# Kernel tuning notes

Measured on AMD Instinct MI355X. Metric: run time of the kernel, lower is better.

## Reference

```python
import jax, jax.numpy as jnp
import numpy as np

N_NODES = 100000
N_EDGES = 3200000
F_IN, HID, N_CLS = 512, 16, 40


def setup_inputs() -> dict:
    key = jax.random.key(0)
    ks = jax.random.split(key, 7)
    x = jax.random.normal(ks[0], (N_NODES, F_IN), dtype=jnp.float32)
    edge_index = jax.random.randint(ks[1], (2, N_EDGES), 0, N_NODES, dtype=jnp.int32)
    edge_weight = jax.random.uniform(ks[2], (N_EDGES,), dtype=jnp.float32)
    # Glorot-style init like PyG's Linear inside GCNConv
    W1 = jax.random.normal(ks[3], (F_IN, HID), dtype=jnp.float32) * (1.0 / np.sqrt(F_IN))
    b1 = jnp.zeros((HID,), dtype=jnp.float32)
    W2 = jax.random.normal(ks[4], (HID, N_CLS), dtype=jnp.float32) * (1.0 / np.sqrt(HID))
    b2 = jnp.zeros((N_CLS,), dtype=jnp.float32)
    return {"x": x, "edge_index": edge_index, "edge_weight": edge_weight,
            "W1": W1, "b1": b1, "W2": W2, "b2": b2}


def reference(x, edge_index, edge_weight, W1, b1, W2, b2):
    N = x.shape[0]
    src, dst = edge_index[0], edge_index[1]
    # add self-loops with weight 1 (GCNConv default add_self_loops=True)
    loop = jnp.arange(N, dtype=edge_index.dtype)
    src_f = jnp.concatenate([src, loop])
    dst_f = jnp.concatenate([dst, loop])
    ew_f = jnp.concatenate([edge_weight, jnp.ones((N,), dtype=edge_weight.dtype)])
    # symmetric normalization: deg computed over target nodes (source_to_target flow)
    deg = jax.ops.segment_sum(ew_f, dst_f, num_segments=N)
    dis = jnp.where(deg > 0, jax.lax.rsqrt(jnp.where(deg > 0, deg, 1.0)), 0.0)
    norm = dis[src_f] * ew_f * dis[dst_f]  # [E+N]

    def conv(h, W, b):
        h = h @ W  # linear before propagate, as in PyG GCNConv
        msg = h[src_f] * norm[:, None]  # [E+N, d_out]
        agg = jax.ops.segment_sum(msg, dst_f, num_segments=N)
        return agg + b

    h = jax.nn.relu(conv(x, W1, b1))
    # dropout is identity in eval mode
    out = conv(h, W2, b2)
    return jax.nn.log_softmax(out, axis=1)
```

## Files before the change

kernel.cpp:

```cpp
#include <hip/hip_runtime.h>
#include <hip/hip_bf16.h>

constexpr int F_IN  = 512;
constexpr int HID   = 16;
constexpr int NCLS  = 40;
constexpr int CHUNK = 4096;
constexpr int BMAX  = 800;
constexpr int SMAX  = 6144;

__device__ __forceinline__ unsigned packEdge(int s, float w) {
  __hip_bfloat16 h = __float2bfloat16(w);
  unsigned short hb = *reinterpret_cast<unsigned short*>(&h);
  return ((unsigned)s << 15) | (unsigned)(hb & 0x7fff);
}
__device__ __forceinline__ float edgeW(unsigned p) {
  return __uint_as_float((p & 0x7fffu) << 16);
}

__global__ void k_scanA(const int* __restrict__ a, int* __restrict__ bsum, int valid) {
  __shared__ int sd[256];
  int t = threadIdx.x;
  int i4 = blockIdx.x * 256 + t;
  int4 v = reinterpret_cast<const int4*>(a)[i4];
  int base = i4 * 4;
  int s = ((base + 0 < valid) ? v.x : 0) + ((base + 1 < valid) ? v.y : 0) +
          ((base + 2 < valid) ? v.z : 0) + ((base + 3 < valid) ? v.w : 0);
  sd[t] = s; __syncthreads();
  for (int off = 128; off > 0; off >>= 1) {
    if (t < off) sd[t] += sd[t + off];
    __syncthreads();
  }
  if (!t) bsum[blockIdx.x] = sd[0];
}

__global__ void k_scanB(int* __restrict__ bsum, int nb) {
  __shared__ int sd[1024];
  int t = threadIdx.x;
  int v = (t < nb) ? bsum[t] : 0;
  sd[t] = v;
  __syncthreads();
  for (int off = 1; off < 1024; off <<= 1) {
    int add = (t >= off) ? sd[t - off] : 0;
    __syncthreads();
    sd[t] += add;
    __syncthreads();
  }
  if (t < nb) bsum[t] = sd[t] - v;
}

__global__ void k_scanC(int* __restrict__ a, const int* __restrict__ bsum, int valid) {
  __shared__ int sd[256];
  int t = threadIdx.x;
  int i4 = blockIdx.x * 256 + t;
  int4 v = reinterpret_cast<int4*>(a)[i4];
  int base = i4 * 4;
  int vx = (base + 0 < valid) ? v.x : 0;
  int vy = (base + 1 < valid) ? v.y : 0;
  int vz = (base + 2 < valid) ? v.z : 0;
  int vw = (base + 3 < valid) ? v.w : 0;
  int ts = vx + vy + vz + vw;
  sd[t] = ts;
  __syncthreads();
  for (int off = 1; off < 256; off <<= 1) {
    int add = (t >= off) ? sd[t - off] : 0;
    __syncthreads();
    sd[t] += add;
    __syncthreads();
  }
  int pre = bsum[blockIdx.x] + sd[t] - ts;
  int4 w;
  w.x = pre; w.y = pre + vx; w.z = w.y + vy; w.w = w.z + vz;
  reinterpret_cast<int4*>(a)[i4] = w;
}

__global__ void __launch_bounds__(256)
k_scat2(const int* __restrict__ src, const int* __restrict__ dst,
        const float* __restrict__ ew, unsigned* __restrict__ payloadA,
        unsigned char* __restrict__ dlowA, int* __restrict__ segs,
        int* __restrict__ counts, int E, int NB, int NBLK) {
  __shared__ unsigned ebuf32[CHUNK];
  __shared__ unsigned char ebufd[CHUNK];
  __shared__ int hist[1024];
  __shared__ int sc[256];
  int t = threadIdx.x;
  int c = blockIdx.x;
  int cbase = c * CHUNK;
  int sz = min(CHUNK, E - cbase);
#pragma unroll
  for (int i = 0; i < 4; ++i) hist[t + 256 * i] = 0;
  __syncthreads();
  unsigned pk[16];
  unsigned char dl[16];
  int key[16];
#pragma unroll
  for (int r = 0; r < 16; ++r) {
    int i = r * 256 + t;
    int e = cbase + i;
    if (i < sz) {
      int s = src[e], d = dst[e];
      pk[r] = packEdge(s, ew[e]);
      dl[r] = (unsigned char)(d & 127);
      key[r] = d >> 7;
      atomicAdd(&hist[key[r]], 1);
    } else {
      key[r] = -1;
    }
  }
  __syncthreads();
  int h0 = hist[4 * t], h1 = hist[4 * t + 1], h2 = hist[4 * t + 2], h3 = hist[4 * t + 3];
  int tsum = h0 + h1 + h2 + h3;
  sc[t] = tsum;
  __syncthreads();
  for (int off = 1; off < 256; off <<= 1) {
    int add = (t >= off) ? sc[t - off] : 0;
    __syncthreads();
    sc[t] += add;
    __syncthreads();
  }
  int pre = sc[t] - tsum;
  __syncthreads();
  hist[4 * t]     = pre;
  hist[4 * t + 1] = pre + h0;
  hist[4 * t + 2] = pre + h0 + h1;
  hist[4 * t + 3] = pre + h0 + h1 + h2;
  __syncthreads();
  size_t sb = (size_t)c * (NB + 1);
  for (int b = t; b < NB; b += 256) {
    int lo = hist[b];
    segs[sb + b] = lo;
    counts[b * NBLK + c] = hist[b + 1] - lo;
  }
  if (t == 0) segs[sb + NB] = sz;
  __syncthreads();
#pragma unroll
  for (int r = 0; r < 16; ++r) {
    if (key[r] >= 0) {
      int pos = atomicAdd(&hist[key[r]], 1);
      ebuf32[pos] = pk[r];
      ebufd[pos]  = dl[r];
    }
  }
  __syncthreads();
  for (int i = t; i < sz; i += 256) {
    payloadA[cbase + i] = ebuf32[i];
    dlowA[cbase + i]    = ebufd[i];
  }
}

__global__ void __launch_bounds__(256)
k_sortb2(const unsigned* __restrict__ payloadA, const unsigned char* __restrict__ dlowA,
         const int* __restrict__ segs, const int* __restrict__ cnts,
         unsigned* __restrict__ payloadB, int* __restrict__ rs,
         float* __restrict__ dis, int N, int NB, int NBLK) {
  __shared__ unsigned ebuf32[SMAX];
  __shared__ unsigned char ebufd[SMAX];
  __shared__ int hcnt[128];
  __shared__ int scn[128];
  __shared__ float dgs[128];
  int t = threadIdx.x;
  int b = blockIdx.x;
  if (t < 128) { hcnt[t] = 0; dgs[t] = 1.0f; }
  __syncthreads();
  int beg = cnts[b * NBLK];
  int end = cnts[b * NBLK + NBLK];
  for (int c = t; c < NBLK; c += 256) {
    int rel = cnts[b * NBLK + c] - beg;
    size_t sb = (size_t)c * (NB + 1) + b;
    int s0 = segs[sb], s1 = segs[sb + 1];
    int gsrc = c * CHUNK + s0;
    for (int k = 0; k < s1 - s0; ++k) {
      unsigned p = payloadA[gsrc + k];
      unsigned char d8 = dlowA[gsrc + k];
      ebuf32[rel + k] = p;
      ebufd[rel + k]  = d8;
      atomicAdd(&hcnt[d8], 1);
      atomicAdd(&dgs[d8], edgeW(p));
    }
  }
  __syncthreads();
  int v = (t < 128) ? hcnt[t] : 0;
  if (t < 128) scn[t] = v;
  __syncthreads();
  for (int off = 1; off < 128; off <<= 1) {
    int add = (t < 128 && t >= off) ? scn[t - off] : 0;
    __syncthreads();
    if (t < 128) scn[t] += add;
    __syncthreads();
  }
  int base = b * 128;
  if (t < 128) {
    int st = scn[t] - v;
    hcnt[t] = st;
    rs[base + t] = beg + st;
    int n = base + t;
    if (n < N) dis[n] = rsqrtf(dgs[t]);
  }
  if (t == 0) rs[base + 128] = end;
  __syncthreads();
  int sz = end - beg;
  for (int i = t; i < sz; i += 256) {
    int pos = beg + atomicAdd(&hcnt[ebufd[i]], 1);
    payloadB[pos] = ebuf32[i];
  }
}

__device__ __forceinline__ float blo(unsigned u) { return __uint_as_float(u << 16); }
__device__ __forceinline__ float bhi(unsigned u) { return __uint_as_float(u & 0xffff0000u); }
__device__ __forceinline__ unsigned pack2(float lo, float hi) {
  __hip_bfloat16 l = __float2bfloat16(lo), h = __float2bfloat16(hi);
  unsigned short ul = *reinterpret_cast<unsigned short*>(&l);
  unsigned short uh = *reinterpret_cast<unsigned short*>(&h);
  return (unsigned)ul | ((unsigned)uh << 16);
}

__global__ void __launch_bounds__(256)
k_gemm1f(const float* __restrict__ x, const float* __restrict__ W1,
         const float* __restrict__ dis, uint4* __restrict__ hb1, int N) {
  __shared__ unsigned xs[4352];
  int t = threadIdx.x;
  int nb = blockIdx.x * 64;
  int r = t & 63;
  int sId = __builtin_amdgcn_readfirstlane(t >> 6);
  float2 acc[8];
#pragma unroll
  for (int j2 = 0; j2 < 8; ++j2) acc[j2] = make_float2(0.f, 0.f);

  float4 ld0, ld1, ld2, ld3, ld4, ld5, ld6, ld7;
#define G1F_LOAD(c)                                                          \
  do {                                                                       \
    int f;                                                                   \
    f = t;           { int row = f >> 5, sl = f & 31; int n = nb + row;      \
      ld0 = (n < N) ? *reinterpret_cast<const float4*>(x + (size_t)n * F_IN + (c) * 128 + sl * 4) : make_float4(0,0,0,0); } \
    f = t + 256;     { int row = f >> 5, sl = f & 31; int n = nb + row;      \
      ld1 = (n < N) ? *reinterpret_cast<const float4*>(x + (size_t)n * F_IN + (c) * 128 + sl * 4) : make_float4(0,0,0,0); } \
    f = t + 512;     { int row = f >> 5, sl = f & 31; int n = nb + row;      \
      ld2 = (n < N) ? *reinterpret_cast<const float4*>(x + (size_t)n * F_IN + (c) * 128 + sl * 4) : make_float4(0,0,0,0); } \
    f = t + 768;     { int row = f >> 5, sl = f & 31; int n = nb + row;      \
      ld3 = (n < N) ? *reinterpret_cast<const float4*>(x + (size_t)n * F_IN + (c) * 128 + sl * 4) : make_float4(0,0,0,0); } \
    f = t + 1024;    { int row = f >> 5, sl = f & 31; int n = nb + row;      \
      ld4 = (n < N) ? *reinterpret_cast<const float4*>(x + (size_t)n * F_IN + (c) * 128 + sl * 4) : make_float4(0,0,0,0); } \
    f = t + 1280;    { int row = f >> 5, sl = f & 31; int n = nb + row;      \
      ld5 = (n < N) ? *reinterpret_cast<const float4*>(x + (size_t)n * F_IN + (c) * 128 + sl * 4) : make_float4(0,0,0,0); } \
    f = t + 1536;    { int row = f >> 5, sl = f & 31; int n = nb + row;      \
      ld6 = (n < N) ? *reinterpret_cast<const float4*>(x + (size_t)n * F_IN + (c) * 128 + sl * 4) : make_float4(0,0,0,0); } \
    f = t + 1792;    { int row = f >> 5, sl = f & 31; int n = nb + row;      \
      ld7 = (n < N) ? *reinterpret_cast<const float4*>(x + (size_t)n * F_IN + (c) * 128 + sl * 4) : make_float4(0,0,0,0); } \
  } while (0)
#define G1F_STORE()                                                          \
  do {                                                                       \
    int f;                                                                   \
    f = t;        { int row = f >> 5, sl = f & 31; int w = row * 65 + sl * 2; \
      xs[w] = pack2(ld0.x, ld0.y); xs[w + 1] = pack2(ld0.z, ld0.w); }        \
    f = t + 256;  { int row = f >> 5, sl = f & 31; int w = row * 65 + sl * 2; \
      xs[w] = pack2(ld1.x, ld1.y); xs[w + 1] = pack2(ld1.z, ld1.w); }        \
    f = t + 512;  { int row = f >> 5, sl = f & 31; int w = row * 65 + sl * 2; \
      xs[w] = pack2(ld2.x, ld2.y); xs[w + 1] = pack2(ld2.z, ld2.w); }        \
    f = t + 768;  { int row = f >> 5, sl = f & 31; int w = row * 65 + sl * 2; \
      xs[w] = pack2(ld3.x, ld3.y); xs[w + 1] = pack2(ld3.z, ld3.w); }        \
    f = t + 1024; { int row = f >> 5, sl = f & 31; int w = row * 65 + sl * 2; \
      xs[w] = pack2(ld4.x, ld4.y); xs[w + 1] = pack2(ld4.z, ld4.w); }        \
    f = t + 1280; { int row = f >> 5, sl = f & 31; int w = row * 65 + sl * 2; \
      xs[w] = pack2(ld5.x, ld5.y); xs[w + 1] = pack2(ld5.z, ld5.w); }        \
    f = t + 1536; { int row = f >> 5, sl = f & 31; int w = row * 65 + sl * 2; \
      xs[w] = pack2(ld6.x, ld6.y); xs[w + 1] = pack2(ld6.z, ld6.w); }        \
    f = t + 1792; { int row = f >> 5, sl = f & 31; int w = row * 65 + sl * 2; \
      xs[w] = pack2(ld7.x, ld7.y); xs[w + 1] = pack2(ld7.z, ld7.w); }        \
  } while (0)

  G1F_LOAD(0);

#pragma unroll
  for (int c = 0; c < 4; ++c) {
    __syncthreads();
    G1F_STORE();
    if (c < 3) G1F_LOAD(c + 1);
    __syncthreads();
    {
      const unsigned* xcol = &xs[r * 65 + sId * 16];
      const float* wbase = W1 + (size_t)(c * 128 + sId * 32) * HID;
#pragma unroll
      for (int mm = 0; mm < 16; ++mm) {
        unsigned u = xcol[mm];
        float x0 = blo(u), x1 = bhi(u);
        const float* w0 = wbase + mm * 32;
        const float* w1 = w0 + HID;
#pragma unroll
        for (int j2 = 0; j2 < 8; ++j2) {
          float2 p0 = *reinterpret_cast<const float2*>(w0 + 2 * j2);
          float2 p1 = *reinterpret_cast<const float2*>(w1 + 2 * j2);
          acc[j2].x = fmaf(x1, p1.x, fmaf(x0, p0.x, acc[j2].x));
          acc[j2].y = fmaf(x1, p1.y, fmaf(x0, p0.y, acc[j2].y));
        }
      }
    }
  }

  __syncthreads();
  float* ps = reinterpret_cast<float*>(xs);
#pragma unroll
  for (int j2 = 0; j2 < 8; ++j2) {
    ps[(sId * 64 + r) * 17 + 2 * j2]     = acc[j2].x;
    ps[(sId * 64 + r) * 17 + 2 * j2 + 1] = acc[j2].y;
  }
  __syncthreads();
  if (t < 64) {
    int n = nb + t;
    if (n < N) {
      float di = dis[n];
      float o[HID];
#pragma unroll
      for (int j = 0; j < HID; ++j)
        o[j] = (ps[t * 17 + j] + ps[(64 + t) * 17 + j] +
                ps[(128 + t) * 17 + j] + ps[(192 + t) * 17 + j]) * di;
      uint4 w0, w1;
      w0.x = pack2(o[0],  o[1]);  w0.y = pack2(o[2],  o[3]);
      w0.z = pack2(o[4],  o[5]);  w0.w = pack2(o[6],  o[7]);
      w1.x = pack2(o[8],  o[9]);  w1.y = pack2(o[10], o[11]);
      w1.z = pack2(o[12], o[13]); w1.w = pack2(o[14], o[15]);
      hb1[(size_t)n * 2]     = w0;
      hb1[(size_t)n * 2 + 1] = w1;
    }
  }
#undef G1F_LOAD
#undef G1F_STORE
}

template <int LAYER>
__global__ void __launch_bounds__(256)
k_aggn8(const unsigned* __restrict__ payload, const int* __restrict__ rs,
        const uint4* __restrict__ hb, const float* __restrict__ dis,
        const float* __restrict__ b1, uint4* __restrict__ hb2,
        const float* __restrict__ W2, const float* __restrict__ b2,
        float* __restrict__ out, int N) {
  int tid = blockIdx.x * 256 + threadIdx.x;
  int n = tid >> 3;
  int q = tid & 7;
  if (n >= N) return;
  int e0 = rs[n], e1 = rs[n + 1];
  float a0 = 0, a1 = 0, a2 = 0, a3 = 0, a4 = 0, a5 = 0, a6 = 0, a7 = 0;
  float a8 = 0, a9 = 0, a10 = 0, a11 = 0, a12 = 0, a13 = 0, a14 = 0, a15 = 0;
  for (int e = e0 + q; e < e1; e += 8) {
    unsigned p = payload[e];
    const uint4* row = hb + ((size_t)(p >> 15) * 2);
    uint4 r0 = row[0];
    uint4 r1 = row[1];
    float w = edgeW(p);
    a0  = fmaf(blo(r0.x), w, a0);  a1  = fmaf(bhi(r0.x), w, a1);
    a2  = fmaf(blo(r0.y), w, a2);  a3  = fmaf(bhi(r0.y), w, a3);
    a4  = fmaf(blo(r0.z), w, a4);  a5  = fmaf(bhi(r0.z), w, a5);
    a6  = fmaf(blo(r0.w), w, a6);  a7  = fmaf(bhi(r0.w), w, a7);
    a8  = fmaf(blo(r1.x), w, a8);  a9  = fmaf(bhi(r1.x), w, a9);
    a10 = fmaf(blo(r1.y), w, a10); a11 = fmaf(bhi(r1.y), w, a11);
    a12 = fmaf(blo(r1.z), w, a12); a13 = fmaf(bhi(r1.z), w, a13);
    a14 = fmaf(blo(r1.w), w, a14); a15 = fmaf(bhi(r1.w), w, a15);
  }
#pragma unroll
  for (int m = 1; m <= 4; m <<= 1) {
    a0  += __shfl_xor(a0,  m); a1  += __shfl_xor(a1,  m);
    a2  += __shfl_xor(a2,  m); a3  += __shfl_xor(a3,  m);
    a4  += __shfl_xor(a4,  m); a5  += __shfl_xor(a5,  m);
    a6  += __shfl_xor(a6,  m); a7  += __shfl_xor(a7,  m);
    a8  += __shfl_xor(a8,  m); a9  += __shfl_xor(a9,  m);
    a10 += __shfl_xor(a10, m); a11 += __shfl_xor(a11, m);
    a12 += __shfl_xor(a12, m); a13 += __shfl_xor(a13, m);
    a14 += __shfl_xor(a14, m); a15 += __shfl_xor(a15, m);
  }
  uint4 s0 = hb[(size_t)n * 2];
  uint4 s1 = hb[(size_t)n * 2 + 1];
  float di = dis[n];
  a0  = (a0  + blo(s0.x)) * di;  a1  = (a1  + bhi(s0.x)) * di;
  a2  = (a2  + blo(s0.y)) * di;  a3  = (a3  + bhi(s0.y)) * di;
  a4  = (a4  + blo(s0.z)) * di;  a5  = (a5  + bhi(s0.z)) * di;
  a6  = (a6  + blo(s0.w)) * di;  a7  = (a7  + bhi(s0.w)) * di;
  a8  = (a8  + blo(s1.x)) * di;  a9  = (a9  + bhi(s1.x)) * di;
  a10 = (a10 + blo(s1.y)) * di;  a11 = (a11 + bhi(s1.y)) * di;
  a12 = (a12 + blo(s1.z)) * di;  a13 = (a13 + bhi(s1.z)) * di;
  a14 = (a14 + blo(s1.w)) * di;  a15 = (a15 + bhi(s1.w)) * di;
  if (LAYER == 1) {
    a0  = fmaxf(a0  + b1[0],  0.0f) * di;  a1  = fmaxf(a1  + b1[1],  0.0f) * di;
    a2  = fmaxf(a2  + b1[2],  0.0f) * di;  a3  = fmaxf(a3  + b1[3],  0.0f) * di;
    a4  = fmaxf(a4  + b1[4],  0.0f) * di;  a5  = fmaxf(a5  + b1[5],  0.0f) * di;
    a6  = fmaxf(a6  + b1[6],  0.0f) * di;  a7  = fmaxf(a7  + b1[7],  0.0f) * di;
    a8  = fmaxf(a8  + b1[8],  0.0f) * di;  a9  = fmaxf(a9  + b1[9],  0.0f) * di;
    a10 = fmaxf(a10 + b1[10], 0.0f) * di;  a11 = fmaxf(a11 + b1[11], 0.0f) * di;
    a12 = fmaxf(a12 + b1[12], 0.0f) * di;  a13 = fmaxf(a13 + b1[13], 0.0f) * di;
    a14 = fmaxf(a14 + b1[14], 0.0f) * di;  a15 = fmaxf(a15 + b1[15], 0.0f) * di;
    if (q == 0) {
      uint4 w0;
      w0.x = pack2(a0, a1);  w0.y = pack2(a2,  a3);
      w0.z = pack2(a4, a5);  w0.w = pack2(a6,  a7);
      hb2[(size_t)n * 2] = w0;
    } else if (q == 1) {
      uint4 w1;
      w1.x = pack2(a8,  a9);  w1.y = pack2(a10, a11);
      w1.z = pack2(a12, a13); w1.w = pack2(a14, a15);
      hb2[(size_t)n * 2 + 1] = w1;
    }
  } else {
    float gv[16] = {a0, a1, a2, a3, a4, a5, a6, a7,
                    a8, a9, a10, a11, a12, a13, a14, a15};
    float o[5];
#pragma unroll
    for (int cc = 0; cc < 5; ++cc) o[cc] = b2[q * 5 + cc];
#pragma unroll
    for (int j = 0; j < HID; ++j) {
      float gj = gv[j];
      const float* wr = W2 + j * NCLS + q * 5;
#pragma unroll
      for (int cc = 0; cc < 5; ++cc) o[cc] = fmaf(gj, wr[cc], o[cc]);
    }
    float m = o[0];
#pragma unroll
    for (int cc = 1; cc < 5; ++cc) m = fmaxf(m, o[cc]);
    m = fmaxf(m, __shfl_xor(m, 1));
    m = fmaxf(m, __shfl_xor(m, 2));
    m = fmaxf(m, __shfl_xor(m, 4));
    float ss = 0.0f;
#pragma unroll
    for (int cc = 0; cc < 5; ++cc) ss += expf(o[cc] - m);
    ss += __shfl_xor(ss, 1);
    ss += __shfl_xor(ss, 2);
    ss += __shfl_xor(ss, 4);
    float lse = m + logf(ss);
    float* orow = out + (size_t)n * NCLS + q * 5;
#pragma unroll
    for (int cc = 0; cc < 5; ++cc) orow[cc] = o[cc] - lse;
  }
}

extern "C" void kernel_launch(void* const* d_in, const int* in_sizes, int n_in,
                              void* d_out, int out_size, void* d_ws, size_t ws_size,
                              hipStream_t stream) {
  const float* x  = (const float*)d_in[0];
  const int*   ei = (const int*)d_in[1];
  const float* ew = (const float*)d_in[2];
  const float* W1 = (const float*)d_in[3];
  const float* b1 = (const float*)d_in[4];
  const float* W2 = (const float*)d_in[5];
  const float* b2 = (const float*)d_in[6];
  float* out = (float*)d_out;

  const int N = in_sizes[0] / F_IN;
  const int E = in_sizes[2];
  const int* src = ei;
  const int* dst = ei + E;

  const int NB   = (N + 127) >> 7;
  const int NBLK = (E + CHUNK - 1) / CHUNK;
  const long long SCT = (long long)NB * NBLK + 1;
  const int Npad = (int)((SCT + 1023) & ~1023LL);
  const int nbScan = Npad / 1024;
  const int Nr   = (NB * 128 + 256 + 255) & ~255;
  const size_t SEGSZ = (size_t)NBLK * (NB + 1) + 4;
  const int valid = NB * NBLK;

  int* counts = (int*)d_ws;
  int* bsum   = counts + Npad;
  float* dis  = (float*)(bsum + 1024);
  int* rs     = (int*)(dis + Nr);
  uint4* hb1  = (uint4*)(rs + Nr);
  uint4* hb2  = hb1 + (size_t)N * 2;
  unsigned* payloadA = (unsigned*)(hb2 + (size_t)N * 2);
  unsigned char* dlowA = (unsigned char*)(payloadA + (size_t)E);
  int* segs   = (int*)(dlowA + (((size_t)E + 3) & ~3ull));
  unsigned* payloadB = (unsigned*)(segs + SEGSZ);

  k_scat2<<<NBLK, 256, 0, stream>>>(src, dst, ew, payloadA, dlowA, segs, counts, E, NB, NBLK);
  k_scanA<<<nbScan, 256, 0, stream>>>(counts, bsum, valid);
  k_scanB<<<1, 1024, 0, stream>>>(bsum, nbScan);
  k_scanC<<<nbScan, 256, 0, stream>>>(counts, bsum, valid);
  k_sortb2<<<NB, 256, 0, stream>>>(payloadA, dlowA, segs, counts, payloadB, rs, dis, N, NB, NBLK);
  k_gemm1f<<<(N + 63) / 64, 256, 0, stream>>>(x, W1, dis, hb1, N);
  const int gAgg = (N * 8 + 255) / 256;
  k_aggn8<1><<<gAgg, 256, 0, stream>>>(payloadB, rs, hb1, dis, b1, hb2,
                                       nullptr, nullptr, nullptr, N);
  k_aggn8<2><<<gAgg, 256, 0, stream>>>(payloadB, rs, hb2, dis, nullptr, nullptr,
                                       W2, b2, out, N);
}
```

Measured before the change: 205.0 us.

## Rewrite first-layer GEMM as single-wave kernel with async global-to-LDS double buffering

```diff
diff --git a/kernel.cpp b/kernel.cpp
--- a/kernel.cpp
+++ b/kernel.cpp
@@ -213,116 +213,67 @@
   return (unsigned)ul | ((unsigned)uh << 16);
 }
 
-__global__ void __launch_bounds__(256)
-k_gemm1f(const float* __restrict__ x, const float* __restrict__ W1,
+#define WAITVM(n) __builtin_amdgcn_s_waitcnt(0x0f70 | (n))
+
+__global__ void __launch_bounds__(64)
+k_gemm1h(const float* __restrict__ x, const float* __restrict__ W1,
          const float* __restrict__ dis, uint4* __restrict__ hb1, int N) {
-  __shared__ unsigned xs[4352];
-  int t = threadIdx.x;
-  int nb = blockIdx.x * 64;
-  int r = t & 63;
-  int sId = __builtin_amdgcn_readfirstlane(t >> 6);
-  float2 acc[8];
-#pragma unroll
-  for (int j2 = 0; j2 < 8; ++j2) acc[j2] = make_float2(0.f, 0.f);
-
-  float4 ld0, ld1, ld2, ld3, ld4, ld5, ld6, ld7;
-#define G1F_LOAD(c)                                                          \
-  do {                                                                       \
-    int f;                                                                   \
-    f = t;           { int row = f >> 5, sl = f & 31; int n = nb + row;      \
-      ld0 = (n < N) ? *reinterpret_cast<const float4*>(x + (size_t)n * F_IN + (c) * 128 + sl * 4) : make_float4(0,0,0,0); } \
-    f = t + 256;     { int row = f >> 5, sl = f & 31; int n = nb + row;      \
-      ld1 = (n < N) ? *reinterpret_cast<const float4*>(x + (size_t)n * F_IN + (c) * 128 + sl * 4) : make_float4(0,0,0,0); } \
-    f = t + 512;     { int row = f >> 5, sl = f & 31; int n = nb + row;      \
-      ld2 = (n < N) ? *reinterpret_cast<const float4*>(x + (size_t)n * F_IN + (c) * 128 + sl * 4) : make_float4(0,0,0,0); } \
-    f = t + 768;     { int row = f >> 5, sl = f & 31; int n = nb + row;      \
-      ld3 = (n < N) ? *reinterpret_cast<const float4*>(x + (size_t)n * F_IN + (c) * 128 + sl * 4) : make_float4(0,0,0,0); } \
-    f = t + 1024;    { int row = f >> 5, sl = f & 31; int n = nb + row;      \
-      ld4 = (n < N) ? *reinterpret_cast<const float4*>(x + (size_t)n * F_IN + (c) * 128 + sl * 4) : make_float4(0,0,0,0); } \
-    f = t + 1280;    { int row = f >> 5, sl = f & 31; int n = nb + row;      \
-      ld5 = (n < N) ? *reinterpret_cast<const float4*>(x + (size_t)n * F_IN + (c) * 128 + sl * 4) : make_float4(0,0,0,0); } \
-    f = t + 1536;    { int row = f >> 5, sl = f & 31; int n = nb + row;      \
-      ld6 = (n < N) ? *reinterpret_cast<const float4*>(x + (size_t)n * F_IN + (c) * 128 + sl * 4) : make_float4(0,0,0,0); } \
-    f = t + 1792;    { int row = f >> 5, sl = f & 31; int n = nb + row;      \
-      ld7 = (n < N) ? *reinterpret_cast<const float4*>(x + (size_t)n * F_IN + (c) * 128 + sl * 4) : make_float4(0,0,0,0); } \
-  } while (0)
-#define G1F_STORE()                                                          \
-  do {                                                                       \
-    int f;                                                                   \
-    f = t;        { int row = f >> 5, sl = f & 31; int w = row * 65 + sl * 2; \
-      xs[w] = pack2(ld0.x, ld0.y); xs[w + 1] = pack2(ld0.z, ld0.w); }        \
-    f = t + 256;  { int row = f >> 5, sl = f & 31; int w = row * 65 + sl * 2; \
-      xs[w] = pack2(ld1.x, ld1.y); xs[w + 1] = pack2(ld1.z, ld1.w); }        \
-    f = t + 512;  { int row = f >> 5, sl = f & 31; int w = row * 65 + sl * 2; \
-      xs[w] = pack2(ld2.x, ld2.y); xs[w + 1] = pack2(ld2.z, ld2.w); }        \
-    f = t + 768;  { int row = f >> 5, sl = f & 31; int w = row * 65 + sl * 2; \
-      xs[w] = pack2(ld3.x, ld3.y); xs[w + 1] = pack2(ld3.z, ld3.w); }        \
-    f = t + 1024; { int row = f >> 5, sl = f & 31; int w = row * 65 + sl * 2; \
-      xs[w] = pack2(ld4.x, ld4.y); xs[w + 1] = pack2(ld4.z, ld4.w); }        \
-    f = t + 1280; { int row = f >> 5, sl = f & 31; int w = row * 65 + sl * 2; \
-      xs[w] = pack2(ld5.x, ld5.y); xs[w + 1] = pack2(ld5.z, ld5.w); }        \
-    f = t + 1536; { int row = f >> 5, sl = f & 31; int w = row * 65 + sl * 2; \
-      xs[w] = pack2(ld6.x, ld6.y); xs[w + 1] = pack2(ld6.z, ld6.w); }        \
-    f = t + 1792; { int row = f >> 5, sl = f & 31; int w = row * 65 + sl * 2; \
-      xs[w] = pack2(ld7.x, ld7.y); xs[w + 1] = pack2(ld7.z, ld7.w); }        \
-  } while (0)
-
-  G1F_LOAD(0);
-
-#pragma unroll
-  for (int c = 0; c < 4; ++c) {
-    __syncthreads();
-    G1F_STORE();
-    if (c < 3) G1F_LOAD(c + 1);
-    __syncthreads();
-    {
-      const unsigned* xcol = &xs[r * 65 + sId * 16];
-      const float* wbase = W1 + (size_t)(c * 128 + sId * 32) * HID;
-#pragma unroll
-      for (int mm = 0; mm < 16; ++mm) {
-        unsigned u = xcol[mm];
-        float x0 = blo(u), x1 = bhi(u);
-        const float* w0 = wbase + mm * 32;
-        const float* w1 = w0 + HID;
-#pragma unroll
-        for (int j2 = 0; j2 < 8; ++j2) {
-          float2 p0 = *reinterpret_cast<const float2*>(w0 + 2 * j2);
-          float2 p1 = *reinterpret_cast<const float2*>(w1 + 2 * j2);
-          acc[j2].x = fmaf(x1, p1.x, fmaf(x0, p0.x, acc[j2].x));
-          acc[j2].y = fmaf(x1, p1.y, fmaf(x0, p0.y, acc[j2].y));
-        }
+  __shared__ float xs[2][1024];
+  const int l = threadIdx.x;
+  const int nb = blockIdx.x * 64;
+  const int q  = (l & 3) ^ ((l >> 3) & 3);
+  const int fr = (l >> 1) & 3;
+  float acc[HID];
+#pragma unroll
+  for (int j = 0; j < HID; ++j) acc[j] = 0.f;
+
+  auto issue = [&](int c, int b) {
+#pragma unroll
+    for (int i = 0; i < 4; ++i) {
+      int row = nb + 16 * i + (l >> 2);
+      if (row >= N) row = N - 1;
+      const float* gp = x + (size_t)row * F_IN + c * 16 + q * 4;
+      __builtin_amdgcn_global_load_lds(
+          (const __attribute__((address_space(1))) unsigned*)(const void*)gp,
+          (__attribute__((address_space(3))) unsigned*)(void*)&xs[b][i * 256],
+          16, 0, 0);
+    }
+  };
+
+  issue(0, 0);
+  issue(1, 1);
+  for (int c = 0; c < 32; ++c) {
+    if (c < 31) WAITVM(4); else WAITVM(0);
+    __builtin_amdgcn_sched_barrier(0);
+    const float* xb = xs[c & 1];
+    const float* wb = W1 + (size_t)(c * 16) * HID;
+#pragma unroll
+    for (int m = 0; m < 4; ++m) {
+      int slot = l * 4 + (m ^ fr);
+      float4 xv = reinterpret_cast<const float4*>(xb)[slot];
+      const float* w0 = wb + (m * 4) * HID;
+#pragma unroll
+      for (int j = 0; j < HID; ++j) {
+        acc[j] = fmaf(xv.x, w0[j], acc[j]);
+        acc[j] = fmaf(xv.y, w0[HID + j], acc[j]);
+        acc[j] = fmaf(xv.z, w0[2 * HID + j], acc[j]);
+        acc[j] = fmaf(xv.w, w0[3 * HID + j], acc[j]);
       }
     }
-  }
-
-  __syncthreads();
-  float* ps = reinterpret_cast<float*>(xs);
-#pragma unroll
-  for (int j2 = 0; j2 < 8; ++j2) {
-    ps[(sId * 64 + r) * 17 + 2 * j2]     = acc[j2].x;
-    ps[(sId * 64 + r) * 17 + 2 * j2 + 1] = acc[j2].y;
-  }
-  __syncthreads();
-  if (t < 64) {
-    int n = nb + t;
-    if (n < N) {
-      float di = dis[n];
-      float o[HID];
-#pragma unroll
-      for (int j = 0; j < HID; ++j)
-        o[j] = (ps[t * 17 + j] + ps[(64 + t) * 17 + j] +
-                ps[(128 + t) * 17 + j] + ps[(192 + t) * 17 + j]) * di;
-      uint4 w0, w1;
-      w0.x = pack2(o[0],  o[1]);  w0.y = pack2(o[2],  o[3]);
-      w0.z = pack2(o[4],  o[5]);  w0.w = pack2(o[6],  o[7]);
-      w1.x = pack2(o[8],  o[9]);  w1.y = pack2(o[10], o[11]);
-      w1.z = pack2(o[12], o[13]); w1.w = pack2(o[14], o[15]);
-      hb1[(size_t)n * 2]     = w0;
-      hb1[(size_t)n * 2 + 1] = w1;
-    }
-  }
-#undef G1F_LOAD
-#undef G1F_STORE
+    __builtin_amdgcn_sched_barrier(0);
+    if (c < 30) issue(c + 2, c & 1);
+  }
+  int n = nb + l;
+  if (n < N) {
+    float di = dis[n];
+    uint4 w0, w1;
+    w0.x = pack2(acc[0] * di,  acc[1] * di);  w0.y = pack2(acc[2] * di,  acc[3] * di);
+    w0.z = pack2(acc[4] * di,  acc[5] * di);  w0.w = pack2(acc[6] * di,  acc[7] * di);
+    w1.x = pack2(acc[8] * di,  acc[9] * di);  w1.y = pack2(acc[10] * di, acc[11] * di);
+    w1.z = pack2(acc[12] * di, acc[13] * di); w1.w = pack2(acc[14] * di, acc[15] * di);
+    hb1[(size_t)n * 2]     = w0;
+    hb1[(size_t)n * 2 + 1] = w1;
+  }
 }
 
 template <int LAYER>
@@ -470,7 +421,7 @@
   k_scanB<<<1, 1024, 0, stream>>>(bsum, nbScan);
   k_scanC<<<nbScan, 256, 0, stream>>>(counts, bsum, valid);
   k_sortb2<<<NB, 256, 0, stream>>>(payloadA, dlowA, segs, counts, payloadB, rs, dis, N, NB, NBLK);
-  k_gemm1f<<<(N + 63) / 64, 256, 0, stream>>>(x, W1, dis, hb1, N);
+  k_gemm1h<<<(N + 63) / 64, 64, 0, stream>>>(x, W1, dis, hb1, N);
   const int gAgg = (N * 8 + 255) / 256;
   k_aggn8<1><<<gAgg, 256, 0, stream>>>(payloadB, rs, hb1, dis, b1, hb2,
                                        nullptr, nullptr, nullptr, N);
```

Result: slower. 209.3 us (+2.1%).
